# Kernel optimization log

Measured on AMD Instinct MI355X. Metric: run time of the kernel, lower is better.

The kernel has to match this reference:

```python
import jax, jax.numpy as jnp
import numpy as np
import math

B, S, D, H = 4, 2048, 1024, 16
DH = D // H  # 64

def setup_inputs() -> dict:
    key = jax.random.key(0)
    ks = jax.random.split(key, 6)
    return {
        "x": jax.random.normal(ks[0], (B, S, D), dtype=jnp.float32),
        "alibi": jax.random.normal(ks[1], (1, H, S, S), dtype=jnp.float32),
        "w_qkv": jax.random.normal(ks[2], (3 * D, D), dtype=jnp.float32) * 0.02,
        "b_qkv": jax.random.normal(ks[3], (3 * D,), dtype=jnp.float32) * 0.02,
        "w_o": jax.random.normal(ks[4], (D, D), dtype=jnp.float32) * 0.02,
        "b_o": jax.random.normal(ks[5], (D,), dtype=jnp.float32) * 0.02,
    }

def reference(x, alibi, w_qkv, b_qkv, w_o, b_o):
    b, s, d = x.shape
    # torch Linear: y = x @ W.T + b
    qkv = x @ w_qkv.T + b_qkv                       # [B, S, 3D]
    qkv = qkv.reshape(b, s, H, 3, DH)               # interleaved per-head q,k,v
    q = jnp.swapaxes(qkv[:, :, :, 0, :], 1, 2)      # [B, H, S, DH]
    k = jnp.swapaxes(qkv[:, :, :, 1, :], 1, 2)
    v = jnp.swapaxes(qkv[:, :, :, 2, :], 1, 2)
    scores = jnp.einsum("bhqd,bhkd->bhqk", q, k) / math.sqrt(DH)
    attn = jax.nn.softmax(scores + alibi, axis=-1)  # [B, H, S, S]
    o = jnp.einsum("bhqk,bhkd->bhqd", attn, v)      # [B, H, S, DH]
    o = jnp.swapaxes(o, 1, 2).reshape(b, s, d)      # [B, S, D]
    return o @ w_o.T + b_o
```

## Files before the change

### kernel.cpp

```cpp
#include <hip/hip_runtime.h>
#include <stdint.h>

#define S_LEN 2048
#define NH    16
#define NB    4
#define DH    64
#define DMODEL 1024

using bf16x8 = __attribute__((ext_vector_type(8))) __bf16;
using f32x4  = __attribute__((ext_vector_type(4))) float;
using us8    = __attribute__((ext_vector_type(8))) unsigned short;

__device__ __forceinline__ unsigned short f2bf_rne(float f) {
    unsigned u = __builtin_bit_cast(unsigned, f);
    return (unsigned short)((u + 0x7FFFu + ((u >> 16) & 1u)) >> 16);
}

__device__ __forceinline__ bf16x8 ld_bf8(const unsigned short* p) {
    return __builtin_bit_cast(bf16x8, *(const us8*)p);
}

__device__ __forceinline__ f32x4 mfma16(bf16x8 a, bf16x8 b, f32x4 c) {
    return __builtin_amdgcn_mfma_f32_16x16x32_bf16(a, b, c, 0, 0, 0);
}

__device__ __forceinline__ float fast_exp2(float x) {
#if __has_builtin(__builtin_amdgcn_exp2f)
    return __builtin_amdgcn_exp2f(x);
#else
    return __expf(x * 0.69314718056f);
#endif
}

typedef __attribute__((address_space(1))) void* gp1_t;
typedef __attribute__((address_space(3))) void* lp3_t;

__device__ __forceinline__ void gload_lds16(const void* g, void* l) {
    __builtin_amdgcn_global_load_lds((gp1_t)(const_cast<void*>(g)), (lp3_t)l, 16, 0, 0);
}

__global__ void cvt_bf16(const float* __restrict__ in, unsigned short* __restrict__ out, int n4) {
    int i = blockIdx.x * 256 + threadIdx.x;
    if (i < n4) {
        float4 v = ((const float4*)in)[i];
        ushort4 o;
        o.x = f2bf_rne(v.x); o.y = f2bf_rne(v.y);
        o.z = f2bf_rne(v.z); o.w = f2bf_rne(v.w);
        ((ushort4*)out)[i] = o;
    }
}

template <int EPI>
__global__ __launch_bounds__(256) void gemm128(
    const unsigned short* __restrict__ A,
    const unsigned short* __restrict__ W,
    const float* __restrict__ bias,
    float* __restrict__ outF,
    unsigned short* __restrict__ Qb,
    unsigned short* __restrict__ Kb,
    unsigned short* __restrict__ Vt,
    int nTilesN)
{
    __shared__ __align__(16) unsigned short As[128 * 32];
    __shared__ __align__(16) unsigned short Bs[128 * 32];

    const int bm = blockIdx.x / nTilesN;
    const int bn = blockIdx.x % nTilesN;
    const int tileM = bm * 128, tileN = bn * 128;
    const int tid = threadIdx.x, lane = tid & 63, w = tid >> 6;
    const int m16 = lane & 15, quad = lane >> 4;
    const int wm = w >> 1, wn = w & 1;

    f32x4 acc[4][4] = {};

    const int c0 = w * 64 + lane;
    const int r0 = c0 >> 2, k0 = (c0 & 3) * 8;
    const int c1 = (4 + w) * 64 + lane;
    const int r1 = c1 >> 2, k1 = (c1 & 3) * 8;

    const unsigned short* Ag0 = A + (size_t)(tileM + r0) * 1024 + k0;
    const unsigned short* Ag1 = A + (size_t)(tileM + r1) * 1024 + k1;
    const unsigned short* Bg0 = W + (size_t)(tileN + r0) * 1024 + k0;
    const unsigned short* Bg1 = W + (size_t)(tileN + r1) * 1024 + k1;
    unsigned short* lA0 = &As[w * 512];
    unsigned short* lA1 = &As[(4 + w) * 512];
    unsigned short* lB0 = &Bs[w * 512];
    unsigned short* lB1 = &Bs[(4 + w) * 512];

    for (int kk = 0; kk < 1024; kk += 32) {
        gload_lds16(Ag0 + kk, lA0);
        gload_lds16(Ag1 + kk, lA1);
        gload_lds16(Bg0 + kk, lB0);
        gload_lds16(Bg1 + kk, lB1);
        __syncthreads();

        bf16x8 af[4], bf[4];
#pragma unroll
        for (int i = 0; i < 4; i++)
            af[i] = ld_bf8(&As[(wm * 64 + i * 16 + m16) * 32 + quad * 8]);
#pragma unroll
        for (int j = 0; j < 4; j++)
            bf[j] = ld_bf8(&Bs[(wn * 64 + j * 16 + m16) * 32 + quad * 8]);
#pragma unroll
        for (int i = 0; i < 4; i++)
#pragma unroll
            for (int j = 0; j < 4; j++)
                acc[i][j] = mfma16(af[i], bf[j], acc[i][j]);
        __syncthreads();
    }

#pragma unroll
    for (int i = 0; i < 4; i++) {
        const int mrow = tileM + wm * 64 + i * 16 + quad * 4;
#pragma unroll
        for (int j = 0; j < 4; j++) {
            const int nb0 = tileN + wn * 64 + j * 16;
            const int n = nb0 + m16;
            const float bv = bias[n];
            if (EPI == 0) {
                const int hh = nb0 / 192, rem = nb0 % 192;
                const int t = rem / 64, dbase = rem % 64;
                const int d = dbase + m16;
#pragma unroll
                for (int r = 0; r < 4; r++) {
                    float val = acc[i][j][r] + bv;
                    const int m = mrow + r;
                    const int b_ = m >> 11, s_ = m & 2047;
                    const size_t bh = (size_t)b_ * NH + hh;
                    if (t == 0)
                        Qb[(bh * S_LEN + s_) * DH + d] = f2bf_rne(val * 0.18033688f);
                    else if (t == 1)
                        Kb[(bh * S_LEN + s_) * DH + d] = f2bf_rne(val);
                    else
                        Vt[(bh * DH + d) * S_LEN + s_] = f2bf_rne(val);
                }
            } else {
#pragma unroll
                for (int r = 0; r < 4; r++) {
                    const int m = mrow + r;
                    outF[(size_t)m * DMODEL + n] = acc[i][j][r] + bv;
                }
            }
        }
    }
}

__global__ __launch_bounds__(256, 4) void attn(const unsigned short* __restrict__ Qb,
                                               const unsigned short* __restrict__ Kb,
                                               const unsigned short* __restrict__ Vt,
                                               const float* __restrict__ alibi,
                                               unsigned short* __restrict__ ob) {
    const int blk = blockIdx.x;
    const int xcd = blk & 7;
    const int b_  = (blk >> 3) & 3;
    const int hq  = xcd * 32 + (blk >> 5);
    const int hh  = hq >> 4, qt = hq & 15;
    const int tid = threadIdx.x, lane = tid & 63, w = tid >> 6;
    const int m16 = lane & 15, quad = lane >> 4;
    const int q0 = qt * 128;
    const size_t bh = (size_t)b_ * NH + hh;

    const unsigned short* Qp = Qb + (bh * S_LEN) * DH;
    const unsigned short* Kp = Kb + bh * S_LEN * DH;
    const unsigned short* Vp = Vt + bh * DH * S_LEN;

    __shared__ __align__(16) unsigned short Ks[128 * 64];
    __shared__ __align__(16) unsigned short Vs[64 * 128];
    __shared__ __align__(16) unsigned int   Pl[4][16 * 20];

    bf16x8 qfrag[2][2];
#pragma unroll
    for (int qf = 0; qf < 2; qf++) {
        const unsigned short* qp = Qp + (size_t)(q0 + w * 32 + qf * 16 + m16) * DH + quad * 8;
        qfrag[qf][0] = ld_bf8(qp);
        qfrag[qf][1] = ld_bf8(qp + 32);
    }
    const float* Apq[2];
#pragma unroll
    for (int qf = 0; qf < 2; qf++)
        Apq[qf] = alibi + ((size_t)hh * S_LEN + q0 + w * 32 + qf * 16 + m16) * S_LEN + quad * 4;

    int offk[4], offv[4];
#pragma unroll
    for (int t = 0; t < 4; t++) {
        const int ck = (w * 4 + t) * 64 + lane;
        const int rk = ck >> 3;
        offk[t] = rk * DH + ((ck & 7) ^ (rk & 7)) * 8;
        const int cv = ck;
        const int dv = cv >> 4;
        offv[t] = dv * S_LEN + ((cv & 15) ^ (dv & 15)) * 8;
    }

    const bf16x8 onesf = __builtin_bit_cast(bf16x8, (us8)(0x3F80u));
    f32x4 oacc[2][4] = {};
    f32x4 ssum[2] = {};
    unsigned int* plw = &Pl[w][0];
    const int sA = m16 & 7;

    float4 alc0 = *(const float4*)(Apq[0]);
    float4 alc1 = *(const float4*)(Apq[0] + 16);

    for (int kc = 0; kc < S_LEN; kc += 128) {
        __syncthreads();
#pragma unroll
        for (int t = 0; t < 4; t++)
            gload_lds16(Kp + (size_t)kc * DH + offk[t], &Ks[(w * 4 + t) * 512]);
#pragma unroll
        for (int t = 0; t < 4; t++)
            gload_lds16(Vp + kc + offv[t], &Vs[(w * 4 + t) * 512]);
        __syncthreads();

#pragma unroll
        for (int qf = 0; qf < 2; qf++) {
            const bf16x8 qa = qfrag[qf][0], qb2 = qfrag[qf][1];
#pragma unroll
            for (int kc2 = 0; kc2 < 4; kc2++) {
                const float* nptr = (kc2 < 3) ? (Apq[qf] + kc + (kc2 + 1) * 32)
                                  : (qf == 0) ? (Apq[1] + kc)
                                              : (Apq[0] + ((kc + 128) & (S_LEN - 1)));
                const float4 aln0 = *(const float4*)(nptr);
                const float4 aln1 = *(const float4*)(nptr + 16);

                f32x4 sc[2];
                __builtin_amdgcn_s_setprio(1);
#pragma unroll
                for (int t = 0; t < 2; t++) {
                    const int krow = (kc2 * 2 + t) * 16 + m16;
                    f32x4 z = {};
                    z = mfma16(ld_bf8(&Ks[krow * DH + (quad ^ sA) * 8]), qa, z);
                    z = mfma16(ld_bf8(&Ks[krow * DH + ((quad + 4) ^ sA) * 8]), qb2, z);
                    sc[t] = z;
                }
                __builtin_amdgcn_s_setprio(0);
#pragma unroll
                for (int t = 0; t < 2; t++) {
                    const float4 av = (t == 0) ? alc0 : alc1;
                    float p0 = fast_exp2(__builtin_fmaf(av.x, 1.44269504f, sc[t][0]));
                    float p1 = fast_exp2(__builtin_fmaf(av.y, 1.44269504f, sc[t][1]));
                    float p2 = fast_exp2(__builtin_fmaf(av.z, 1.44269504f, sc[t][2]));
                    float p3 = fast_exp2(__builtin_fmaf(av.w, 1.44269504f, sc[t][3]));
                    uint2 pk;
                    pk.x = (__builtin_bit_cast(unsigned, p0) >> 16) |
                           (__builtin_bit_cast(unsigned, p1) & 0xFFFF0000u);
                    pk.y = (__builtin_bit_cast(unsigned, p2) >> 16) |
                           (__builtin_bit_cast(unsigned, p3) & 0xFFFF0000u);
                    *(uint2*)&plw[m16 * 20 + t * 8 + quad * 2] = pk;
                }
                const bf16x8 pf = ld_bf8((const unsigned short*)&plw[m16 * 20 + quad * 4]);
                __builtin_amdgcn_s_setprio(1);
                ssum[qf] = mfma16(pf, onesf, ssum[qf]);
#pragma unroll
                for (int db = 0; db < 4; db++) {
                    const int vrow = db * 16 + m16;
                    const bf16x8 vf = ld_bf8(&Vs[vrow * 128 + ((kc2 * 4 + quad) ^ m16) * 8]);
                    oacc[qf][db] = mfma16(pf, vf, oacc[qf][db]);
                }
                __builtin_amdgcn_s_setprio(0);

                alc0 = aln0;
                alc1 = aln1;
            }
        }
    }

#pragma unroll
    for (int qf = 0; qf < 2; qf++) {
        f32x4 rinv;
#pragma unroll
        for (int r = 0; r < 4; r++) rinv[r] = 1.0f / ssum[qf][r];
#pragma unroll
        for (int db = 0; db < 4; db++)
#pragma unroll
            for (int r = 0; r < 4; r++) {
                const int q = q0 + w * 32 + qf * 16 + quad * 4 + r;
                ob[((size_t)b_ * S_LEN + q) * DMODEL + hh * DH + db * 16 + m16] =
                    f2bf_rne(oacc[qf][db][r] * rinv[r]);
            }
    }
}

extern "C" void kernel_launch(void* const* d_in, const int* in_sizes, int n_in,
                              void* d_out, int out_size, void* d_ws, size_t ws_size,
                              hipStream_t stream) {
    (void)in_sizes; (void)n_in; (void)out_size; (void)ws_size;
    const float* x      = (const float*)d_in[0];
    const float* alibi  = (const float*)d_in[1];
    const float* w_qkv  = (const float*)d_in[2];
    const float* b_qkv  = (const float*)d_in[3];
    const float* w_o    = (const float*)d_in[4];
    const float* b_o    = (const float*)d_in[5];
    float* out = (float*)d_out;

    char* ws = (char*)d_ws;
    unsigned short* xb    = (unsigned short*)(ws);
    unsigned short* wqkvb = (unsigned short*)(ws + 16777216);
    unsigned short* wob   = (unsigned short*)(ws + 23068672);
    unsigned short* Qb    = (unsigned short*)(ws + 25165824);
    unsigned short* Kb    = (unsigned short*)(ws + 41943040);
    unsigned short* Vt    = (unsigned short*)(ws + 58720256);
    unsigned short* ob    = (unsigned short*)(ws + 75497472);

    cvt_bf16<<<8192, 256, 0, stream>>>(x, xb, 8388608 / 4);
    cvt_bf16<<<3072, 256, 0, stream>>>(w_qkv, wqkvb, 3145728 / 4);
    cvt_bf16<<<1024, 256, 0, stream>>>(w_o, wob, 1048576 / 4);

    gemm128<0><<<64 * 24, 256, 0, stream>>>(xb, wqkvb, b_qkv, nullptr, Qb, Kb, Vt, 24);
    attn<<<1024, 256, 0, stream>>>(Qb, Kb, Vt, alibi, ob);
    gemm128<1><<<64 * 8, 256, 0, stream>>>(ob, wob, b_o, out, nullptr, nullptr, nullptr, 8);
}
```

Measured before the change: 598.5 us.

## Rewrite projection GEMMs with 256-row tiles, double-buffered LDS, XOR swizzle

Replaces the 128x128 single-buffered GEMM with a templated 256xBN kernel using 512 threads, BK=64, double-buffered LDS staging via global_load_lds, an XOR-swizzled LDS layout to avoid bank conflicts, and a blockIdx remap for L2 locality. Prefetching the next K slab while computing the current one is meant to hide global-load latency, and the larger tiles raise arithmetic intensity in both the QKV and output projections. In exchange LDS use grows (up to 128 KB per block for BN=256), which limits occupancy, and the grids get smaller (384 and 256 blocks), which may leave CUs underused. The GEMMs are only part of the total time, since attention dominates.

```diff
diff --git a/kernel.cpp b/kernel.cpp
--- a/kernel.cpp
+++ b/kernel.cpp
@@ -38,6 +38,8 @@
 __device__ __forceinline__ void gload_lds16(const void* g, void* l) {
     __builtin_amdgcn_global_load_lds((gp1_t)(const_cast<void*>(g)), (lp3_t)l, 16, 0, 0);
 }
+
+#define VM_BARRIER() asm volatile("s_waitcnt vmcnt(0)\n\ts_barrier" ::: "memory")
 
 __global__ void cvt_bf16(const float* __restrict__ in, unsigned short* __restrict__ out, int n4) {
     int i = blockIdx.x * 256 + threadIdx.x;
@@ -50,8 +52,8 @@
     }
 }
 
-template <int EPI>
-__global__ __launch_bounds__(256) void gemm128(
+template <int EPI, int BN>
+__global__ __launch_bounds__(512, 2) void gemm256(
     const unsigned short* __restrict__ A,
     const unsigned short* __restrict__ W,
     const float* __restrict__ bias,
@@ -61,59 +63,92 @@
     unsigned short* __restrict__ Vt,
     int nTilesN)
 {
-    __shared__ __align__(16) unsigned short As[128 * 32];
-    __shared__ __align__(16) unsigned short Bs[128 * 32];
-
-    const int bm = blockIdx.x / nTilesN;
-    const int bn = blockIdx.x % nTilesN;
-    const int tileM = bm * 128, tileN = bn * 128;
+    constexpr int BM = 256, BK = 64;
+    constexpr int WGN = BN / 64;
+    constexpr int WM  = BM / (8 / WGN);
+    constexpr int MI  = WM / 16;
+    constexpr int NJ  = 4;
+    constexpr int AI  = (BM * BK / 8) / 512;
+    constexpr int BI  = (BN * BK / 8) / 512;
+
+    __shared__ __align__(16) unsigned short As[2][BM * BK];
+    __shared__ __align__(16) unsigned short Bs[2][BN * BK];
+
+    const int nwg = gridDim.x;
+    const int swz = (blockIdx.x & 7) * (nwg >> 3) + (blockIdx.x >> 3);
+    const int bm = swz / nTilesN;
+    const int bn = swz % nTilesN;
+    const int tileM = bm * BM, tileN = bn * BN;
+
     const int tid = threadIdx.x, lane = tid & 63, w = tid >> 6;
     const int m16 = lane & 15, quad = lane >> 4;
-    const int wm = w >> 1, wn = w & 1;
-
-    f32x4 acc[4][4] = {};
-
-    const int c0 = w * 64 + lane;
-    const int r0 = c0 >> 2, k0 = (c0 & 3) * 8;
-    const int c1 = (4 + w) * 64 + lane;
-    const int r1 = c1 >> 2, k1 = (c1 & 3) * 8;
-
-    const unsigned short* Ag0 = A + (size_t)(tileM + r0) * 1024 + k0;
-    const unsigned short* Ag1 = A + (size_t)(tileM + r1) * 1024 + k1;
-    const unsigned short* Bg0 = W + (size_t)(tileN + r0) * 1024 + k0;
-    const unsigned short* Bg1 = W + (size_t)(tileN + r1) * 1024 + k1;
-    unsigned short* lA0 = &As[w * 512];
-    unsigned short* lA1 = &As[(4 + w) * 512];
-    unsigned short* lB0 = &Bs[w * 512];
-    unsigned short* lB1 = &Bs[(4 + w) * 512];
-
-    for (int kk = 0; kk < 1024; kk += 32) {
-        gload_lds16(Ag0 + kk, lA0);
-        gload_lds16(Ag1 + kk, lA1);
-        gload_lds16(Bg0 + kk, lB0);
-        gload_lds16(Bg1 + kk, lB1);
-        __syncthreads();
-
-        bf16x8 af[4], bf[4];
-#pragma unroll
-        for (int i = 0; i < 4; i++)
-            af[i] = ld_bf8(&As[(wm * 64 + i * 16 + m16) * 32 + quad * 8]);
-#pragma unroll
-        for (int j = 0; j < 4; j++)
-            bf[j] = ld_bf8(&Bs[(wn * 64 + j * 16 + m16) * 32 + quad * 8]);
-#pragma unroll
-        for (int i = 0; i < 4; i++)
-#pragma unroll
-            for (int j = 0; j < 4; j++)
-                acc[i][j] = mfma16(af[i], bf[j], acc[i][j]);
-        __syncthreads();
-    }
-
-#pragma unroll
-    for (int i = 0; i < 4; i++) {
-        const int mrow = tileM + wm * 64 + i * 16 + quad * 4;
-#pragma unroll
-        for (int j = 0; j < 4; j++) {
+    const int wm = w / WGN, wn = w % WGN;
+
+    f32x4 acc[MI][NJ] = {};
+
+    size_t aoff[AI], boff[BI];
+#pragma unroll
+    for (int i = 0; i < AI; i++) {
+        const int u = (i * 8 + w) * 64 + lane;
+        const int row = u >> 3, slot = u & 7;
+        aoff[i] = (size_t)(tileM + row) * 1024 + (size_t)((slot ^ (row & 7)) * 8);
+    }
+#pragma unroll
+    for (int i = 0; i < BI; i++) {
+        const int u = (i * 8 + w) * 64 + lane;
+        const int row = u >> 3, slot = u & 7;
+        boff[i] = (size_t)(tileN + row) * 1024 + (size_t)((slot ^ (row & 7)) * 8);
+    }
+
+#define STAGE(buf, kk) do {                                               \
+        _Pragma("unroll")                                                 \
+        for (int i = 0; i < AI; i++)                                      \
+            gload_lds16(A + aoff[i] + (kk), &As[buf][(i * 8 + w) * 512]); \
+        _Pragma("unroll")                                                 \
+        for (int i = 0; i < BI; i++)                                      \
+            gload_lds16(W + boff[i] + (kk), &Bs[buf][(i * 8 + w) * 512]); \
+    } while (0)
+
+#define COMPUTE(buf) do {                                                          \
+        _Pragma("unroll")                                                          \
+        for (int ks = 0; ks < 2; ks++) {                                           \
+            bf16x8 af[MI], bfv[NJ];                                                \
+            _Pragma("unroll")                                                      \
+            for (int i = 0; i < MI; i++) {                                         \
+                const int R = wm * WM + i * 16 + m16;                              \
+                af[i] = ld_bf8(&As[buf][(R * 8 + ((ks * 4 + quad) ^ (R & 7))) * 8]); \
+            }                                                                      \
+            _Pragma("unroll")                                                      \
+            for (int j = 0; j < NJ; j++) {                                         \
+                const int Rb = wn * 64 + j * 16 + m16;                             \
+                bfv[j] = ld_bf8(&Bs[buf][(Rb * 8 + ((ks * 4 + quad) ^ (Rb & 7))) * 8]); \
+            }                                                                      \
+            _Pragma("unroll")                                                      \
+            for (int i = 0; i < MI; i++)                                           \
+                _Pragma("unroll")                                                  \
+                for (int j = 0; j < NJ; j++)                                       \
+                    acc[i][j] = mfma16(af[i], bfv[j], acc[i][j]);                  \
+        }                                                                          \
+    } while (0)
+
+    STAGE(0, 0);
+    VM_BARRIER();
+    for (int kk = 0; kk < 1024; kk += 128) {
+        if (kk + 64 < 1024) STAGE(1, kk + 64);
+        COMPUTE(0);
+        VM_BARRIER();
+        if (kk + 128 < 1024) STAGE(0, kk + 128);
+        COMPUTE(1);
+        VM_BARRIER();
+    }
+#undef STAGE
+#undef COMPUTE
+
+#pragma unroll
+    for (int i = 0; i < MI; i++) {
+        const int mrow = tileM + wm * WM + i * 16 + quad * 4;
+#pragma unroll
+        for (int j = 0; j < NJ; j++) {
             const int nb0 = tileN + wn * 64 + j * 16;
             const int n = nb0 + m16;
             const float bv = bias[n];
@@ -304,7 +339,7 @@
     cvt_bf16<<<3072, 256, 0, stream>>>(w_qkv, wqkvb, 3145728 / 4);
     cvt_bf16<<<1024, 256, 0, stream>>>(w_o, wob, 1048576 / 4);
 
-    gemm128<0><<<64 * 24, 256, 0, stream>>>(xb, wqkvb, b_qkv, nullptr, Qb, Kb, Vt, 24);
+    gemm256<0, 256><<<384, 512, 0, stream>>>(xb, wqkvb, b_qkv, nullptr, Qb, Kb, Vt, 12);
     attn<<<1024, 256, 0, stream>>>(Qb, Kb, Vt, alibi, ob);
-    gemm128<1><<<64 * 8, 256, 0, stream>>>(ob, wob, b_o, out, nullptr, nullptr, nullptr, 8);
-}
+    gemm256<1, 128><<<256, 512, 0, stream>>>(ob, wob, b_o, out, nullptr, nullptr, nullptr, 8);
+}
```

Result: no change. 608.4 us (+1.7%).
